# Performance work log

Hardware: AMD Instinct MI355X
Metric: run time of the kernel (lower is better)

## Reference

```python
import jax, jax.numpy as jnp
import numpy as np

B = 16
N = 1024            # num_nodes
U = 64              # num_units
K = 2               # max_diffusion_step
M = K + 1           # num diffusion matrices
F = 2 * U           # inputs + state features per node


def _random_walk(adj):
    # adj: [B, N, N]; faithful to torch: add I, degree = sum over dim 1 (column sums),
    # then diag_embed(d_inv) @ adj (scales rows).
    a = adj + jnp.eye(N, dtype=adj.dtype)
    d = jnp.sum(a, axis=1)                      # [B, N]
    d_inv = jnp.where(d == 0, jnp.zeros_like(d), 1.0 / d)
    return d_inv[:, :, None] * a                # [B, N, N]


def _diffuse(A, x):
    # Faithful reproduction of the torch concat pattern:
    xs = [x]
    if K > 0:
        x1 = jnp.matmul(A, x)
        xs.append(x1)
        for _ in range(2, K + 1):
            x2 = jnp.matmul(A, x1)
            xs.append(x1)
            x1 = x2
    return jnp.stack(xs, axis=-1)               # [B, N, F, M]


def _gconv(inputs, state, A0, A1, W0, b0, W1, b1):
    b = inputs.shape[0]
    x = jnp.concatenate([inputs.reshape(b, N, -1), state.reshape(b, N, -1)], axis=-1)  # [B,N,F]
    f = x.shape[-1]
    x0 = _diffuse(A0, x).reshape(b * N, f * M)
    x1 = _diffuse(A1, x).reshape(b * N, f * M)
    return (x0 @ W0 + b0) + (x1 @ W1 + b1)       # [B*N, out]


def setup_inputs() -> dict:
    key = jax.random.key(0)
    ks = jax.random.split(key, 12)
    din = F * M
    s = 1.0 / np.sqrt(din)
    inputs = jax.random.normal(ks[0], (B, N * U), dtype=jnp.float32)
    hx = jax.random.normal(ks[1], (B, N * U), dtype=jnp.float32)
    adj = jax.random.uniform(ks[2], (B, N, N), dtype=jnp.float32)
    W0 = jax.random.normal(ks[3], (din, 2 * U), dtype=jnp.float32) * s
    b0 = jnp.full((2 * U,), 0.1, dtype=jnp.float32)
    W1 = jax.random.normal(ks[4], (din, 2 * U), dtype=jnp.float32) * s
    b1 = jnp.full((2 * U,), 0.1, dtype=jnp.float32)
    Wc0 = jax.random.normal(ks[5], (din, U), dtype=jnp.float32) * s
    bc0 = jnp.full((U,), 0.1, dtype=jnp.float32)
    Wc1 = jax.random.normal(ks[6], (din, U), dtype=jnp.float32) * s
    bc1 = jnp.full((U,), 0.1, dtype=jnp.float32)
    return {"inputs": inputs, "hx": hx, "adj": adj, "W0": W0, "b0": b0,
            "W1": W1, "b1": b1, "Wc0": Wc0, "bc0": bc0, "Wc1": Wc1, "bc1": bc1}


def reference(inputs, hx, adj, W0, b0, W1, b1, Wc0, bc0, Wc1, bc1):
    b = inputs.shape[0]
    A0 = _random_walk(adj)
    A1 = _random_walk(jnp.transpose(adj, (0, 2, 1)))
    # reset / update gates
    value = jax.nn.sigmoid(_gconv(inputs, hx, A0, A1, W0, b0, W1, b1))  # [B*N, 2U]
    value = value.reshape(b, N, 2 * U)
    r = value[..., :U].reshape(b, N * U)
    u = value[..., U:].reshape(b, N * U)
    # candidate state
    c = _gconv(inputs, r * hx, A0, A1, Wc0, bc0, Wc1, bc1)              # [B*N, U]
    c = jnp.tanh(c).reshape(b, N * U)
    new_state = u * hx + (1.0 - u) * c
    return new_state
```

## Files before the change

kernel.cpp:

```cpp
#include <hip/hip_runtime.h>
#include <hip/hip_bf16.h>

typedef unsigned short u16;
typedef unsigned int u32;
typedef unsigned char u8;
typedef long i64;
typedef __bf16 bf16x8 __attribute__((ext_vector_type(8)));
typedef float floatx4 __attribute__((ext_vector_type(4)));

#define MFMA16(a,b,c) __builtin_amdgcn_mfma_f32_16x16x32_bf16((a),(b),(c),0,0,0)
#define MFMA8(a,b,c)  __builtin_amdgcn_mfma_f32_16x16x32_fp8_fp8((a),(b),(c),0,0,0)
#define AS1 __attribute__((address_space(1)))
#define AS3 __attribute__((address_space(3)))
#define VM6 asm volatile("s_waitcnt vmcnt(6)" ::: "memory")
#define VM4 asm volatile("s_waitcnt vmcnt(4)" ::: "memory")
#define VM3 asm volatile("s_waitcnt vmcnt(3)" ::: "memory")
#define VM2 asm volatile("s_waitcnt vmcnt(2)" ::: "memory")
#define VM0 asm volatile("s_waitcnt vmcnt(0)" ::: "memory")
#define SBAR __builtin_amdgcn_s_barrier()
#define SCHED0 __builtin_amdgcn_sched_barrier(0)

__device__ __forceinline__ void gl16(const void* g, void* l){
  __builtin_amdgcn_global_load_lds((const AS1 void*)g, (AS3 void*)l, 16, 0, 0);
}
__device__ __forceinline__ u16 f2bf(float f){
  u32 u = __builtin_bit_cast(u32, f);
  u += 0x7FFFu + ((u >> 16) & 1u);
  return (u16)(u >> 16);
}
__device__ __forceinline__ float bf2f(u16 h){
  u32 u = ((u32)h) << 16;
  return __builtin_bit_cast(float, u);
}
__device__ __forceinline__ bf16x8 ldfrag(const u16* p){
  return *(const bf16x8*)p;
}
__device__ __forceinline__ u32 pk4(float a, float b, float c, float d){
  int r = __builtin_amdgcn_cvt_pk_fp8_f32(a, b, 0, false);
  r = __builtin_amdgcn_cvt_pk_fp8_f32(c, d, r, true);
  return (u32)r;
}
__device__ __forceinline__ i64 ldA8(const char* chunk, int r, int kf, int lg){
  int sr = r >> 1;
  int G = (((r&1)<<2) + (kf<<1) + (lg>>1)) ^ (sr&7);
  return *(const i64*)(chunk + sr*128 + G*16 + (lg&1)*8);
}

__global__ __launch_bounds__(256) void kp3_prep(
    const float* __restrict__ inp, const float* __restrict__ hx,
    const float* __restrict__ adj,
    const float* __restrict__ W0, const float* __restrict__ b0,
    const float* __restrict__ W1, const float* __restrict__ b1,
    const float* __restrict__ Wc0, const float* __restrict__ bc0,
    const float* __restrict__ Wc1, const float* __restrict__ bc1,
    u16* __restrict__ WgT, u16* __restrict__ WcT,
    float* __restrict__ bias_g, float* __restrict__ bias_c,
    u8* __restrict__ adjf8, u8* __restrict__ adjTf8,
    u8* __restrict__ Xtf8, u16* __restrict__ XC2){
  __shared__ __align__(16) char sh[40960];
  int t = threadIdx.x;
  int blk = blockIdx.x;
  if (blk < 256) {
    float (*XT)[80] = (float(*)[80])sh;
    int r = t >> 2;
    int row = blk*64 + r;
    int fq = t & 3;
    const float4* ip = (const float4*)(inp + (size_t)row*64 + fq*16);
    const float4* hp = (const float4*)(hx  + (size_t)row*64 + fq*16);
    float iv[16], hv[16];
    #pragma unroll
    for (int q=0;q<4;q++){
      float4 a = ip[q]; iv[4*q]=a.x; iv[4*q+1]=a.y; iv[4*q+2]=a.z; iv[4*q+3]=a.w;
      float4 c = hp[q]; hv[4*q]=c.x; hv[4*q+1]=c.y; hv[4*q+2]=c.z; hv[4*q+3]=c.w;
    }
    u32 pi[8];
    #pragma unroll
    for (int q=0;q<8;q++)
      pi[q] = (u32)f2bf(iv[2*q]) | ((u32)f2bf(iv[2*q+1])<<16);
    size_t rbase = (size_t)row*384;
    *(uint4*)(XC2 + rbase + fq*16)     = make_uint4(pi[0],pi[1],pi[2],pi[3]);
    *(uint4*)(XC2 + rbase + fq*16 + 8) = make_uint4(pi[4],pi[5],pi[6],pi[7]);
    #pragma unroll
    for (int q=0;q<16;q++){
      XT[fq*16+q][r]    = iv[q];
      XT[64+fq*16+q][r] = hv[q];
    }
    __syncthreads();
    int feat = t >> 1, half = t & 1;
    int b = blk >> 4, n0 = (blk & 15)*64;
    const float* src = &XT[feat][half*32];
    u32 o[8];
    #pragma unroll
    for (int p=0;p<8;p++)
      o[p] = pk4(src[4*p],src[4*p+1],src[4*p+2],src[4*p+3]);
    u8* dst = Xtf8 + (size_t)b*131072 + (size_t)feat*1024 + n0 + half*32;
    *(uint4*)dst      = make_uint4(o[0],o[1],o[2],o[3]);
    *(uint4*)(dst+16) = make_uint4(o[4],o[5],o[6],o[7]);
    return;
  }
  if (blk < 544) {
    int id = (blk - 256)*256 + t;
    if (id < 128*384) {
      int n = id / 384, k = id % 384;
      float v;
      if (k < 128)       v = W0[(k*3+0)*128 + n] + W1[(k*3+0)*128 + n];
      else if (k < 256){ int f = k-128; v = W0[(f*3+1)*128+n] + W0[(f*3+2)*128+n]; }
      else             { int f = k-256; v = W1[(f*3+1)*128+n] + W1[(f*3+2)*128+n]; }
      WgT[(size_t)n*384 + k] = f2bf(v);
    } else {
      int id2 = id - 128*384;
      int n = id2 / 384, k = id2 % 384;
      float v;
      if (k < 128)       v = Wc0[(k*3+0)*64 + n] + Wc1[(k*3+0)*64 + n];
      else if (k < 256){ int f = k-128; v = Wc0[(f*3+1)*64+n] + Wc0[(f*3+2)*64+n]; }
      else             { int f = k-256; v = Wc1[(f*3+1)*64+n] + Wc1[(f*3+2)*64+n]; }
      WcT[(size_t)n*384 + k] = f2bf(v);
    }
    if (blk == 256) {
      if (t < 128) bias_g[t] = b0[t] + b1[t];
      if (t < 64)  bias_c[t] = bc0[t] + bc1[t];
    }
    return;
  }
  u8* ltb = (u8*)sh;
  int blk2 = blk - 544;
  int b = blk2 >> 6, st = (blk2 >> 2) & 15, h = blk2 & 3;
  int i0 = st*64;
  int r = t >> 2, cq = t & 3;
  size_t base = (size_t)b << 20;
  for (int c = h*4; c < h*4+4; ++c){
    int j0 = c*64, cb = c & 1;
    const float4* s4 = (const float4*)(adj + base + (size_t)(i0 + r)*1024 + j0 + (cq<<4));
    float v[16];
    #pragma unroll
    for (int q = 0; q < 4; q++) {
      float4 f = s4[q];
      v[4*q]=f.x; v[4*q+1]=f.y; v[4*q+2]=f.z; v[4*q+3]=f.w;
    }
    u32 pk[4];
    #pragma unroll
    for (int p = 0; p < 4; p++)
      pk[p] = pk4(v[4*p],v[4*p+1],v[4*p+2],v[4*p+3]);
    *(uint4*)(adjf8 + base + (size_t)(i0 + r)*1024 + j0 + (cq<<4)) =
      make_uint4(pk[0],pk[1],pk[2],pk[3]);
    #pragma unroll
    for (int q = 0; q < 16; q++)
      ltb[cb*4608 + (cq*16+q)*72 + r] = (u8)(pk[q>>2] >> ((q&3)*8));
    __syncthreads();
    u32 w4[4];
    #pragma unroll
    for (int p = 0; p < 4; p++){
      u32 b0v = ltb[cb*4608 + r*72 + cq*16 + 4*p];
      u32 b1v = ltb[cb*4608 + r*72 + cq*16 + 4*p+1];
      u32 b2v = ltb[cb*4608 + r*72 + cq*16 + 4*p+2];
      u32 b3v = ltb[cb*4608 + r*72 + cq*16 + 4*p+3];
      w4[p] = b0v | (b1v<<8) | (b2v<<16) | (b3v<<24);
    }
    *(uint4*)(adjTf8 + base + (size_t)(j0 + r)*1024 + i0 + (cq<<4)) =
      make_uint4(w4[0],w4[1],w4[2],w4[3]);
  }
}

__global__ __launch_bounds__(256) void kg2_gates(
    const u8* __restrict__ adjf8, const u8* __restrict__ adjTf8,
    const u8* __restrict__ Xtf8,
    const float* __restrict__ inp, const float* __restrict__ hx,
    const u16* __restrict__ WgT, const float* __restrict__ bias_g,
    u16* __restrict__ XC2, u8* __restrict__ Stf8, float* __restrict__ uBuf){
  __shared__ __align__(16) char lds[36864];
  int bid = ((blockIdx.x & 7)<<6) + (blockIdx.x >> 3);
  int mt = bid & 31, b = bid >> 5;
  int t = threadIdx.x, w = t>>6, l = t&63, lr = l&15, lg = l>>4;
  int wm = w>>1, wn = w&1;
  int gp = (l&7) ^ ((l>>3)&7);
  size_t off = (size_t)(2*(l>>3) + (gp>>2))*1024 + (gp&3)*16;
  const u8* A0g = adjf8  + ((size_t)b<<20) + (size_t)mt*32768 + off;
  const u8* A1g = adjTf8 + ((size_t)b<<20) + (size_t)mt*32768 + off;
  const u8* Bg  = Xtf8 + (size_t)b*131072 + off;
  floatx4 acc0[4] = {}, acc1[4] = {}, s0 = {}, s1 = {};
  const i64 ONES = 0x3838383838383838L;
  #define STG_KG(bufi, kk) do{ \
    if (w==0){ gl16(A0g+(kk), lds+(bufi)*2048); gl16(A0g+(kk)+16384, lds+(bufi)*2048+1024); gl16(Bg+(kk), lds+12288+(bufi)*8192); } \
    else if (w==1){ gl16(A1g+(kk), lds+6144+(bufi)*2048); gl16(A1g+(kk)+16384, lds+6144+(bufi)*2048+1024); gl16(Bg+(kk)+16384, lds+12288+(bufi)*8192+1024); } \
    else if (w==2){ gl16(Bg+(kk)+32768, lds+12288+(bufi)*8192+2048); gl16(Bg+(kk)+49152, lds+12288+(bufi)*8192+3072); gl16(Bg+(kk)+65536, lds+12288+(bufi)*8192+4096); } \
    else { gl16(Bg+(kk)+81920, lds+12288+(bufi)*8192+5120); gl16(Bg+(kk)+98304, lds+12288+(bufi)*8192+6144); gl16(Bg+(kk)+114688, lds+12288+(bufi)*8192+7168); } \
  }while(0)
  STG_KG(0, 0);
  STG_KG(1, 64);
  int cur = 0;
  for (int step = 0; step < 16; ++step){
    if (step < 14) {
      int nb = cur + 2; if (nb >= 3) nb -= 3;
      STG_KG(nb, (step+2)*64);
      VM6;
    } else if (step == 14) { VM3; } else { VM0; }
    SBAR; SCHED0;
    const char* A0b = lds + cur*2048;
    const char* A1b = lds + 6144 + cur*2048;
    const char* Bb  = lds + 12288 + cur*8192;
    #pragma unroll
    for (int kf=0; kf<2; kf++){
      i64 a0 = ldA8(A0b, wm*16+lr, kf, lg);
      i64 a1 = ldA8(A1b, wm*16+lr, kf, lg);
      s0 = MFMA8(a0, ONES, s0);
      s1 = MFMA8(a1, ONES, s1);
      #pragma unroll
      for (int nf=0; nf<4; nf++){
        i64 bb = ldA8(Bb, wn*64+nf*16+lr, kf, lg);
        acc0[nf] = MFMA8(a0, bb, acc0[nf]);
        acc1[nf] = MFMA8(a1, bb, acc1[nf]);
      }
    }
    SCHED0; SBAR;
    if (++cur == 3) cur = 0;
  }
  __syncthreads();
  u16* SL = (u16*)lds;
  u16* SLT = (u16*)(lds + 25088);
  float d0i[4], d1i[4];
  #pragma unroll
  for (int rr=0; rr<4; rr++){
    d1i[rr] = 1.0f / (s0[rr] + 1.0f);
    d0i[rr] = 1.0f / (s1[rr] + 1.0f);
  }
  #pragma unroll
  for (int nf = 0; nf < 4; nf++) {
    #pragma unroll
    for (int rr = 0; rr < 4; rr++) {
      int rl = wm*16 + lg*4 + rr;
      int row = mt*32 + rl;
      int col = wn*64 + nf*16 + lr;
      float xv = (col < 64) ? inp[(size_t)(b*1024+row)*64 + col]
                            : hx [(size_t)(b*1024+row)*64 + (col-64)];
      float y0 = (acc0[nf][rr] + xv) * d0i[rr];
      float y1 = (acc1[nf][rr] + xv) * d1i[rr];
      u16 b0v = f2bf(y0), b1v = f2bf(y1);
      SL[rl*392 + col]       = f2bf(xv);
      SL[rl*392 + 128 + col] = b0v;
      SL[rl*392 + 256 + col] = b1v;
      if (col < 64) {
        size_t grow = (size_t)(b*1024 + row)*384;
        XC2[grow + 128 + col] = b0v;
        XC2[grow + 256 + col] = b1v;
      }
    }
  }
  __syncthreads();
  floatx4 g[4] = {};
  for (int kk = 0; kk < 384; kk += 32) {
    int ko = kk + lg*8;
    bf16x8 a = ldfrag(&SL[(size_t)(wm*16+lr)*392 + ko]);
    #pragma unroll
    for (int nf = 0; nf < 4; nf++)
      g[nf] = MFMA16(a, ldfrag(WgT + (size_t)(wn*64+nf*16+lr)*384 + ko), g[nf]);
  }
  #pragma unroll
  for (int nf = 0; nf < 4; nf++) {
    #pragma unroll
    for (int rr = 0; rr < 4; rr++) {
      int rl = wm*16 + lg*4 + rr;
      int row = mt*32 + rl;
      int col = wn*64 + nf*16 + lr;
      float pre = g[nf][rr] + bias_g[col];
      float s = 1.0f / (1.0f + __expf(-pre));
      if (col < 64) {
        float shv = s * hx[(size_t)(b*1024+row)*64 + col];
        u16 bv = f2bf(shv);
        XC2[(size_t)(b*1024+row)*384 + 64 + col] = bv;
        SLT[col*40 + rl] = bv;
      } else {
        uBuf[(size_t)(b*1024+row)*64 + (col-64)] = s;
      }
    }
  }
  __syncthreads();
  {
    int c2 = t >> 2, q = t & 3;
    uint4 vv = *(const uint4*)&SLT[c2*40 + q*8];
    u32 arr[4] = {vv.x, vv.y, vv.z, vv.w};
    float f[8];
    #pragma unroll
    for (int e=0;e<8;e++) f[e] = bf2f((u16)(arr[e>>1] >> ((e&1)*16)));
    u32 p0 = pk4(f[0],f[1],f[2],f[3]);
    u32 p1 = pk4(f[4],f[5],f[6],f[7]);
    *(uint2*)(Stf8 + (size_t)b*65536 + (size_t)c2*1024 + mt*32 + q*8) = make_uint2(p0,p1);
  }
  #undef STG_KG
}

__global__ __launch_bounds__(256) void kz2_cand(
    const u8* __restrict__ adjf8, const u8* __restrict__ adjTf8,
    const u8* __restrict__ Stf8,
    const u16* __restrict__ XC2, const u16* __restrict__ WcT,
    const float* __restrict__ bias_c,
    const float* __restrict__ uBuf, const float* __restrict__ hx,
    float* __restrict__ out){
  __shared__ __align__(16) char lds[25088];
  int bid = ((blockIdx.x & 7)<<6) + (blockIdx.x >> 3);
  int mt = bid & 31, b = bid >> 5;
  int t = threadIdx.x, w = t>>6, l = t&63, lr = l&15, lg = l>>4;
  int wm = w>>1, wn = w&1;
  int gp = (l&7) ^ ((l>>3)&7);
  size_t off = (size_t)(2*(l>>3) + (gp>>2))*1024 + (gp&3)*16;
  const u8* A0g = adjf8  + ((size_t)b<<20) + (size_t)mt*32768 + off;
  const u8* A1g = adjTf8 + ((size_t)b<<20) + (size_t)mt*32768 + off;
  const u8* Bg  = Stf8 + (size_t)b*65536 + off;
  floatx4 z0[2] = {}, z1[2] = {}, s0 = {}, s1 = {};
  const i64 ONES = 0x3838383838383838L;
  #define STG_KZ(bufi, kk) do{ \
    if (w==0){ gl16(A0g+(kk), lds+(bufi)*2048); gl16(A0g+(kk)+16384, lds+(bufi)*2048+1024); } \
    else if (w==1){ gl16(A1g+(kk), lds+6144+(bufi)*2048); gl16(A1g+(kk)+16384, lds+6144+(bufi)*2048+1024); } \
    else if (w==2){ gl16(Bg+(kk), lds+12288+(bufi)*4096); gl16(Bg+(kk)+16384, lds+12288+(bufi)*4096+1024); } \
    else { gl16(Bg+(kk)+32768, lds+12288+(bufi)*4096+2048); gl16(Bg+(kk)+49152, lds+12288+(bufi)*4096+3072); } \
  }while(0)
  STG_KZ(0, 0);
  STG_KZ(1, 64);
  int cur = 0;
  for (int step = 0; step < 16; ++step){
    if (step < 14) {
      int nb = cur + 2; if (nb >= 3) nb -= 3;
      STG_KZ(nb, (step+2)*64);
      VM4;
    } else if (step == 14) { VM2; } else { VM0; }
    SBAR; SCHED0;
    const char* A0b = lds + cur*2048;
    const char* A1b = lds + 6144 + cur*2048;
    const char* Bb  = lds + 12288 + cur*4096;
    #pragma unroll
    for (int kf=0; kf<2; kf++){
      i64 a0 = ldA8(A0b, wm*16+lr, kf, lg);
      i64 a1 = ldA8(A1b, wm*16+lr, kf, lg);
      s0 = MFMA8(a0, ONES, s0);
      s1 = MFMA8(a1, ONES, s1);
      #pragma unroll
      for (int nf=0; nf<2; nf++){
        i64 bb = ldA8(Bb, wn*32+nf*16+lr, kf, lg);
        z0[nf] = MFMA8(a0, bb, z0[nf]);
        z1[nf] = MFMA8(a1, bb, z1[nf]);
      }
    }
    SCHED0; SBAR;
    if (++cur == 3) cur = 0;
  }
  __syncthreads();
  u16* SL = (u16*)lds;
  {
    int rl = t >> 3, s = t & 7;
    size_t grow = (size_t)(b*1024 + mt*32 + rl)*384;
    #pragma unroll
    for (int j = 0; j < 3; j++)
      *(uint4*)&SL[(size_t)rl*392 + s*24 + j*8] =
        *(const uint4*)(XC2 + grow + s*24 + j*8);
    *(uint4*)&SL[(size_t)rl*392 + 256 + s*8] =
      *(const uint4*)(XC2 + grow + 256 + s*8);
  }
  float d0i[4], d1i[4];
  #pragma unroll
  for (int rr=0; rr<4; rr++){
    d1i[rr] = 1.0f / (s0[rr] + 1.0f);
    d0i[rr] = 1.0f / (s1[rr] + 1.0f);
  }
  #pragma unroll
  for (int nf = 0; nf < 2; nf++) {
    #pragma unroll
    for (int rr = 0; rr < 4; rr++) {
      int rl = wm*16 + lg*4 + rr;
      int row = mt*32 + rl;
      int col = wn*32 + nf*16 + lr;
      float sval = bf2f(XC2[(size_t)(b*1024+row)*384 + 64 + col]);
      SL[rl*392 + 192 + col] = f2bf((z0[nf][rr] + sval) * d0i[rr]);
      SL[rl*392 + 320 + col] = f2bf((z1[nf][rr] + sval) * d1i[rr]);
    }
  }
  __syncthreads();
  floatx4 c[2] = {};
  for (int kk = 0; kk < 384; kk += 32) {
    int ko = kk + lg*8;
    bf16x8 a = ldfrag(&SL[(size_t)(wm*16+lr)*392 + ko]);
    #pragma unroll
    for (int nf = 0; nf < 2; nf++)
      c[nf] = MFMA16(a, ldfrag(WcT + (size_t)(wn*32+nf*16+lr)*384 + ko), c[nf]);
  }
  #pragma unroll
  for (int nf = 0; nf < 2; nf++) {
    #pragma unroll
    for (int rr = 0; rr < 4; rr++) {
      int row = mt*32 + wm*16 + lg*4 + rr;
      int col = wn*32 + nf*16 + lr;
      float pre = c[nf][rr] + bias_c[col];
      pre = fminf(fmaxf(pre, -15.f), 15.f);
      float e2 = __expf(2.0f*pre);
      float cv = (e2 - 1.0f) / (e2 + 1.0f);
      float u = uBuf[(size_t)(b*1024+row)*64 + col];
      float h = hx[(size_t)(b*1024+row)*64 + col];
      out[(size_t)(b*1024+row)*64 + col] = u*h + (1.0f - u)*cv;
    }
  }
  #undef STG_KZ
}

extern "C" void kernel_launch(void* const* d_in, const int* in_sizes, int n_in,
                              void* d_out, int out_size, void* d_ws, size_t ws_size,
                              hipStream_t stream) {
  (void)in_sizes; (void)n_in; (void)out_size; (void)ws_size;
  const float* inp = (const float*)d_in[0];
  const float* hx  = (const float*)d_in[1];
  const float* adj = (const float*)d_in[2];
  const float* W0  = (const float*)d_in[3];
  const float* b0  = (const float*)d_in[4];
  const float* W1  = (const float*)d_in[5];
  const float* b1  = (const float*)d_in[6];
  const float* Wc0 = (const float*)d_in[7];
  const float* bc0 = (const float*)d_in[8];
  const float* Wc1 = (const float*)d_in[9];
  const float* bc1 = (const float*)d_in[10];
  float* out = (float*)d_out;
  char* ws = (char*)d_ws;

  u8* adjf8   = (u8*)(ws + 0);
  u8* adjTf8  = (u8*)(ws + 16777216);
  u8* Xtf8    = (u8*)(ws + 33554432);
  u16* XC2    = (u16*)(ws + 35651584);
  u8* Stf8    = (u8*)(ws + 48234496);
  float* uBuf = (float*)(ws + 49283072);
  u16* WgT    = (u16*)(ws + 53477376);
  u16* WcT    = (u16*)(ws + 53575680);
  float* bias_g = (float*)(ws + 53624832);
  float* bias_c = (float*)(ws + 53625344);

  hipLaunchKernelGGL(kp3_prep, dim3(1568), dim3(256), 0, stream,
                     inp, hx, adj, W0, b0, W1, b1, Wc0, bc0, Wc1, bc1,
                     WgT, WcT, bias_g, bias_c, adjf8, adjTf8, Xtf8, XC2);
  hipLaunchKernelGGL(kg2_gates, dim3(512), dim3(256), 0, stream,
                     adjf8, adjTf8, Xtf8, inp, hx, WgT, bias_g, XC2, Stf8, uBuf);
  hipLaunchKernelGGL(kz2_cand, dim3(512), dim3(256), 0, stream,
                     adjf8, adjTf8, Stf8, XC2, WcT, bias_c, uBuf, hx, out);
}
```

Measured before the change: 74.83 us.

## Fuse prep, gate and candidate kernels into one cooperative persistent kernel

Replaces the three-launch pipeline (prep, gates, candidate) with one cooperative kernel of 512 blocks that uses grid.sync between phases. Intermediate per-tile data (the concatenated features, the update gate and the r*h values) stays in LDS across phases instead of round-tripping through global buffers such as XC2 and uBuf. This is meant to remove launch gaps and some global traffic. In exchange it adds two grid-wide barriers, requires all 512 blocks to be co-resident (2 per CU under the launch bounds), and falls back to the old three kernels if the cooperative launch fails.

```diff
diff --git a/kernel.cpp b/kernel.cpp
--- a/kernel.cpp
+++ b/kernel.cpp
@@ -1,5 +1,8 @@
 #include <hip/hip_runtime.h>
 #include <hip/hip_bf16.h>
+#include <hip/hip_cooperative_groups.h>
+
+namespace cg = cooperative_groups;
 
 typedef unsigned short u16;
 typedef unsigned int u32;
@@ -44,6 +47,308 @@
   int sr = r >> 1;
   int G = (((r&1)<<2) + (kf<<1) + (lg>>1)) ^ (sr&7);
   return *(const i64*)(chunk + sr*128 + G*16 + (lg&1)*8);
+}
+
+__global__ __launch_bounds__(256, 2) void mega(
+    const float* __restrict__ inp, const float* __restrict__ hx,
+    const float* __restrict__ adj,
+    const float* __restrict__ W0, const float* __restrict__ b0,
+    const float* __restrict__ W1, const float* __restrict__ b1,
+    const float* __restrict__ Wc0, const float* __restrict__ bc0,
+    const float* __restrict__ Wc1, const float* __restrict__ bc1,
+    u16* __restrict__ WgT, u16* __restrict__ WcT,
+    float* __restrict__ bias_g, float* __restrict__ bias_c,
+    u8* __restrict__ adjf8, u8* __restrict__ adjTf8,
+    u8* __restrict__ Xtf8, u8* __restrict__ Stf8,
+    float* __restrict__ out){
+  __shared__ __align__(16) char lds[53888];
+  cg::grid_group grid = cg::this_grid();
+  int t = threadIdx.x;
+  int blk = blockIdx.x;
+
+  if (blk < 256) {
+    float (*XT)[80] = (float(*)[80])lds;
+    int r = t >> 2, fq = t & 3;
+    int row = blk*64 + r;
+    const float4* ip = (const float4*)(inp + (size_t)row*64 + fq*16);
+    const float4* hp = (const float4*)(hx  + (size_t)row*64 + fq*16);
+    float iv[16], hv[16];
+    #pragma unroll
+    for (int q=0;q<4;q++){
+      float4 a = ip[q]; iv[4*q]=a.x; iv[4*q+1]=a.y; iv[4*q+2]=a.z; iv[4*q+3]=a.w;
+      float4 c = hp[q]; hv[4*q]=c.x; hv[4*q+1]=c.y; hv[4*q+2]=c.z; hv[4*q+3]=c.w;
+    }
+    #pragma unroll
+    for (int q=0;q<16;q++){
+      XT[fq*16+q][r]    = iv[q];
+      XT[64+fq*16+q][r] = hv[q];
+    }
+    __syncthreads();
+    int feat = t >> 1, half = t & 1;
+    int bb2 = blk >> 4, n0 = (blk & 15)*64;
+    const float* src = &XT[feat][half*32];
+    u32 o[8];
+    #pragma unroll
+    for (int p=0;p<8;p++)
+      o[p] = pk4(src[4*p],src[4*p+1],src[4*p+2],src[4*p+3]);
+    u8* dst = Xtf8 + (size_t)bb2*131072 + (size_t)feat*1024 + n0 + half*32;
+    *(uint4*)dst      = make_uint4(o[0],o[1],o[2],o[3]);
+    *(uint4*)(dst+16) = make_uint4(o[4],o[5],o[6],o[7]);
+    __syncthreads();
+  }
+  if (blk >= 224) {
+    int id = (blk - 224)*256 + t;
+    if (id < 128*384) {
+      int n = id / 384, k = id % 384;
+      float v;
+      if (k < 128)       v = W0[(k*3+0)*128 + n] + W1[(k*3+0)*128 + n];
+      else if (k < 256){ int f = k-128; v = W0[(f*3+1)*128+n] + W0[(f*3+2)*128+n]; }
+      else             { int f = k-256; v = W1[(f*3+1)*128+n] + W1[(f*3+2)*128+n]; }
+      WgT[(size_t)n*384 + k] = f2bf(v);
+    } else {
+      int id2 = id - 128*384;
+      int n = id2 / 384, k = id2 % 384;
+      float v;
+      if (k < 128)       v = Wc0[(k*3+0)*64 + n] + Wc1[(k*3+0)*64 + n];
+      else if (k < 256){ int f = k-128; v = Wc0[(f*3+1)*64+n] + Wc0[(f*3+2)*64+n]; }
+      else             { int f = k-256; v = Wc1[(f*3+1)*64+n] + Wc1[(f*3+2)*64+n]; }
+      WcT[(size_t)n*384 + k] = f2bf(v);
+    }
+    if (blk == 224) {
+      if (t < 128) bias_g[t] = b0[t] + b1[t];
+      if (t < 64)  bias_c[t] = bc0[t] + bc1[t];
+    }
+  }
+  {
+    u8* ltb = (u8*)lds;
+    int r = t >> 2, cq = t & 3;
+    for (int uu = blk*2; uu < blk*2 + 2; ++uu){
+      int b = uu >> 6, st = (uu >> 2) & 15, h = uu & 3;
+      int i0 = st*64;
+      size_t base = (size_t)b << 20;
+      __syncthreads();
+      for (int c = h*4; c < h*4+4; ++c){
+        int j0 = c*64, cb = c & 1;
+        const float4* s4 = (const float4*)(adj + base + (size_t)(i0 + r)*1024 + j0 + (cq<<4));
+        float v[16];
+        #pragma unroll
+        for (int q = 0; q < 4; q++) {
+          float4 f = s4[q];
+          v[4*q]=f.x; v[4*q+1]=f.y; v[4*q+2]=f.z; v[4*q+3]=f.w;
+        }
+        u32 pk[4];
+        #pragma unroll
+        for (int p = 0; p < 4; p++)
+          pk[p] = pk4(v[4*p],v[4*p+1],v[4*p+2],v[4*p+3]);
+        *(uint4*)(adjf8 + base + (size_t)(i0 + r)*1024 + j0 + (cq<<4)) =
+          make_uint4(pk[0],pk[1],pk[2],pk[3]);
+        #pragma unroll
+        for (int q = 0; q < 16; q++)
+          ltb[cb*4608 + (cq*16+q)*72 + r] = (u8)(pk[q>>2] >> ((q&3)*8));
+        __syncthreads();
+        u32 w4[4];
+        #pragma unroll
+        for (int p = 0; p < 4; p++){
+          u32 b0v = ltb[cb*4608 + r*72 + cq*16 + 4*p];
+          u32 b1v = ltb[cb*4608 + r*72 + cq*16 + 4*p+1];
+          u32 b2v = ltb[cb*4608 + r*72 + cq*16 + 4*p+2];
+          u32 b3v = ltb[cb*4608 + r*72 + cq*16 + 4*p+3];
+          w4[p] = b0v | (b1v<<8) | (b2v<<16) | (b3v<<24);
+        }
+        *(uint4*)(adjTf8 + base + (size_t)(j0 + r)*1024 + i0 + (cq<<4)) =
+          make_uint4(w4[0],w4[1],w4[2],w4[3]);
+      }
+    }
+  }
+  __threadfence();
+  grid.sync();
+
+  int bid = ((blk & 7)<<6) + (blk >> 3);
+  int mt = bid & 31, b = bid >> 5;
+  int w = t>>6, l = t&63, lr = l&15, lg = l>>4;
+  int wm = w>>1, wn = w&1;
+  int gp = (l&7) ^ ((l>>3)&7);
+  size_t off = (size_t)(2*(l>>3) + (gp>>2))*1024 + (gp&3)*16;
+  const u8* A0g = adjf8  + ((size_t)b<<20) + (size_t)mt*32768 + off;
+  const u8* A1g = adjTf8 + ((size_t)b<<20) + (size_t)mt*32768 + off;
+  u16* SL = (u16*)lds;
+  u16* uL = (u16*)(lds + 25088);
+  char* stg = lds + 29312;
+  const i64 ONES = 0x3838383838383838L;
+  float d0i[4], d1i[4];
+
+  {
+    const u8* Bg = Xtf8 + (size_t)b*131072 + off;
+    floatx4 acc0[4] = {}, acc1[4] = {}, s0 = {}, s1 = {};
+    #define STG_G(bi, kk) do{ \
+      if (w==0){ gl16(A0g+(kk), stg+(bi)*2048); gl16(A0g+(kk)+16384, stg+(bi)*2048+1024); gl16(Bg+(kk), stg+8192+(bi)*8192); } \
+      else if (w==1){ gl16(A1g+(kk), stg+4096+(bi)*2048); gl16(A1g+(kk)+16384, stg+4096+(bi)*2048+1024); gl16(Bg+(kk)+16384, stg+8192+(bi)*8192+1024); } \
+      else if (w==2){ gl16(Bg+(kk)+32768, stg+8192+(bi)*8192+2048); gl16(Bg+(kk)+49152, stg+8192+(bi)*8192+3072); gl16(Bg+(kk)+65536, stg+8192+(bi)*8192+4096); } \
+      else { gl16(Bg+(kk)+81920, stg+8192+(bi)*8192+5120); gl16(Bg+(kk)+98304, stg+8192+(bi)*8192+6144); gl16(Bg+(kk)+114688, stg+8192+(bi)*8192+7168); } \
+    }while(0)
+    STG_G(0, 0);
+    int cur = 0;
+    for (int step = 0; step < 16; ++step){
+      if (step < 15) { STG_G(cur^1, (step+1)*64); VM3; } else { VM0; }
+      SBAR; SCHED0;
+      const char* A0b = stg + cur*2048;
+      const char* A1b = stg + 4096 + cur*2048;
+      const char* Bb  = stg + 8192 + cur*8192;
+      #pragma unroll
+      for (int kf=0; kf<2; kf++){
+        i64 a0 = ldA8(A0b, wm*16+lr, kf, lg);
+        i64 a1 = ldA8(A1b, wm*16+lr, kf, lg);
+        s0 = MFMA8(a0, ONES, s0);
+        s1 = MFMA8(a1, ONES, s1);
+        #pragma unroll
+        for (int nf=0; nf<4; nf++){
+          i64 bb = ldA8(Bb, wn*64+nf*16+lr, kf, lg);
+          acc0[nf] = MFMA8(a0, bb, acc0[nf]);
+          acc1[nf] = MFMA8(a1, bb, acc1[nf]);
+        }
+      }
+      SCHED0; SBAR;
+      cur ^= 1;
+    }
+    #undef STG_G
+    __syncthreads();
+    #pragma unroll
+    for (int rr=0; rr<4; rr++){
+      d1i[rr] = 1.0f / (s0[rr] + 1.0f);
+      d0i[rr] = 1.0f / (s1[rr] + 1.0f);
+    }
+    #pragma unroll
+    for (int nf = 0; nf < 4; nf++) {
+      #pragma unroll
+      for (int rr = 0; rr < 4; rr++) {
+        int rl = wm*16 + lg*4 + rr;
+        int row = mt*32 + rl;
+        int col = wn*64 + nf*16 + lr;
+        float xv = (col < 64) ? inp[(size_t)(b*1024+row)*64 + col]
+                              : hx [(size_t)(b*1024+row)*64 + (col-64)];
+        float y0 = (acc0[nf][rr] + xv) * d0i[rr];
+        float y1 = (acc1[nf][rr] + xv) * d1i[rr];
+        SL[rl*392 + col]       = f2bf(xv);
+        SL[rl*392 + 128 + col] = f2bf(y0);
+        SL[rl*392 + 256 + col] = f2bf(y1);
+      }
+    }
+    __syncthreads();
+    floatx4 g[4] = {};
+    for (int kk = 0; kk < 384; kk += 32) {
+      int ko = kk + lg*8;
+      bf16x8 a = ldfrag(&SL[(size_t)(wm*16+lr)*392 + ko]);
+      #pragma unroll
+      for (int nf = 0; nf < 4; nf++)
+        g[nf] = MFMA16(a, ldfrag(WgT + (size_t)(wn*64+nf*16+lr)*384 + ko), g[nf]);
+    }
+    __syncthreads();
+    u16* SLT = (u16*)stg;
+    #pragma unroll
+    for (int nf = 0; nf < 4; nf++) {
+      #pragma unroll
+      for (int rr = 0; rr < 4; rr++) {
+        int rl = wm*16 + lg*4 + rr;
+        int row = mt*32 + rl;
+        int col = wn*64 + nf*16 + lr;
+        float pre = g[nf][rr] + bias_g[col];
+        float s = 1.0f / (1.0f + __expf(-pre));
+        if (col < 64) {
+          float shv = s * hx[(size_t)(b*1024+row)*64 + col];
+          u16 bv = f2bf(shv);
+          SL[rl*392 + 64 + col] = bv;
+          SLT[col*40 + rl] = bv;
+        } else {
+          uL[rl*66 + (col-64)] = f2bf(s);
+        }
+      }
+    }
+    __syncthreads();
+    {
+      int c2 = t >> 2, q = t & 3;
+      uint4 vv = *(const uint4*)&SLT[c2*40 + q*8];
+      u32 arr[4] = {vv.x, vv.y, vv.z, vv.w};
+      float f[8];
+      #pragma unroll
+      for (int e=0;e<8;e++) f[e] = bf2f((u16)(arr[e>>1] >> ((e&1)*16)));
+      u32 p0 = pk4(f[0],f[1],f[2],f[3]);
+      u32 p1 = pk4(f[4],f[5],f[6],f[7]);
+      *(uint2*)(Stf8 + (size_t)b*65536 + (size_t)c2*1024 + mt*32 + q*8) = make_uint2(p0,p1);
+    }
+  }
+  __threadfence();
+  grid.sync();
+
+  {
+    const u8* Bg = Stf8 + (size_t)b*65536 + off;
+    floatx4 z0[2] = {}, z1[2] = {};
+    #define STG_Z(bi, kk) do{ \
+      if (w==0){ gl16(A0g+(kk), stg+(bi)*2048); gl16(A0g+(kk)+16384, stg+(bi)*2048+1024); } \
+      else if (w==1){ gl16(A1g+(kk), stg+4096+(bi)*2048); gl16(A1g+(kk)+16384, stg+4096+(bi)*2048+1024); } \
+      else if (w==2){ gl16(Bg+(kk), stg+8192+(bi)*4096); gl16(Bg+(kk)+16384, stg+8192+(bi)*4096+1024); } \
+      else { gl16(Bg+(kk)+32768, stg+8192+(bi)*4096+2048); gl16(Bg+(kk)+49152, stg+8192+(bi)*4096+3072); } \
+    }while(0)
+    STG_Z(0, 0);
+    int cur = 0;
+    for (int step = 0; step < 16; ++step){
+      if (step < 15) { STG_Z(cur^1, (step+1)*64); VM2; } else { VM0; }
+      SBAR; SCHED0;
+      const char* A0b = stg + cur*2048;
+      const char* A1b = stg + 4096 + cur*2048;
+      const char* Bb  = stg + 8192 + cur*4096;
+      #pragma unroll
+      for (int kf=0; kf<2; kf++){
+        i64 a0 = ldA8(A0b, wm*16+lr, kf, lg);
+        i64 a1 = ldA8(A1b, wm*16+lr, kf, lg);
+        #pragma unroll
+        for (int nf=0; nf<2; nf++){
+          i64 bb = ldA8(Bb, wn*32+nf*16+lr, kf, lg);
+          z0[nf] = MFMA8(a0, bb, z0[nf]);
+          z1[nf] = MFMA8(a1, bb, z1[nf]);
+        }
+      }
+      SCHED0; SBAR;
+      cur ^= 1;
+    }
+    #undef STG_Z
+    __syncthreads();
+    #pragma unroll
+    for (int nf = 0; nf < 2; nf++) {
+      #pragma unroll
+      for (int rr = 0; rr < 4; rr++) {
+        int rl = wm*16 + lg*4 + rr;
+        int col = wn*32 + nf*16 + lr;
+        float sval = bf2f(SL[rl*392 + 64 + col]);
+        SL[rl*392 + 192 + col] = f2bf((z0[nf][rr] + sval) * d0i[rr]);
+        SL[rl*392 + 320 + col] = f2bf((z1[nf][rr] + sval) * d1i[rr]);
+      }
+    }
+    __syncthreads();
+    floatx4 c[2] = {};
+    for (int kk = 0; kk < 384; kk += 32) {
+      int ko = kk + lg*8;
+      bf16x8 a = ldfrag(&SL[(size_t)(wm*16+lr)*392 + ko]);
+      #pragma unroll
+      for (int nf = 0; nf < 2; nf++)
+        c[nf] = MFMA16(a, ldfrag(WcT + (size_t)(wn*32+nf*16+lr)*384 + ko), c[nf]);
+    }
+    #pragma unroll
+    for (int nf = 0; nf < 2; nf++) {
+      #pragma unroll
+      for (int rr = 0; rr < 4; rr++) {
+        int rl = wm*16 + lg*4 + rr;
+        int row = mt*32 + rl;
+        int col = wn*32 + nf*16 + lr;
+        float pre = c[nf][rr] + bias_c[col];
+        pre = fminf(fmaxf(pre, -15.f), 15.f);
+        float e2 = __expf(2.0f*pre);
+        float cv = (e2 - 1.0f) / (e2 + 1.0f);
+        float u = bf2f(uL[rl*66 + col]);
+        float h = hx[(size_t)(b*1024+row)*64 + col];
+        out[(size_t)(b*1024+row)*64 + col] = u*h + (1.0f - u)*cv;
+      }
+    }
+  }
 }
 
 __global__ __launch_bounds__(256) void kp3_prep(
@@ -62,9 +367,8 @@
   int blk = blockIdx.x;
   if (blk < 256) {
     float (*XT)[80] = (float(*)[80])sh;
-    int r = t >> 2;
+    int r = t >> 2, fq = t & 3;
     int row = blk*64 + r;
-    int fq = t & 3;
     const float4* ip = (const float4*)(inp + (size_t)row*64 + fq*16);
     const float4* hp = (const float4*)(hx  + (size_t)row*64 + fq*16);
     float iv[16], hv[16];
@@ -428,11 +732,18 @@
   float* bias_g = (float*)(ws + 53624832);
   float* bias_c = (float*)(ws + 53625344);
 
-  hipLaunchKernelGGL(kp3_prep, dim3(1568), dim3(256), 0, stream,
-                     inp, hx, adj, W0, b0, W1, b1, Wc0, bc0, Wc1, bc1,
-                     WgT, WcT, bias_g, bias_c, adjf8, adjTf8, Xtf8, XC2);
-  hipLaunchKernelGGL(kg2_gates, dim3(512), dim3(256), 0, stream,
-                     adjf8, adjTf8, Xtf8, inp, hx, WgT, bias_g, XC2, Stf8, uBuf);
-  hipLaunchKernelGGL(kz2_cand, dim3(512), dim3(256), 0, stream,
-                     adjf8, adjTf8, Stf8, XC2, WcT, bias_c, uBuf, hx, out);
-}
+  void* args[] = {&inp, &hx, &adj, &W0, &b0, &W1, &b1, &Wc0, &bc0, &Wc1, &bc1,
+                  &WgT, &WcT, &bias_g, &bias_c, &adjf8, &adjTf8, &Xtf8, &Stf8,
+                  &out};
+  hipError_t e = hipLaunchCooperativeKernel((void*)mega, dim3(512), dim3(256),
+                                            args, 0, stream);
+  if (e != hipSuccess) {
+    hipLaunchKernelGGL(kp3_prep, dim3(1568), dim3(256), 0, stream,
+                       inp, hx, adj, W0, b0, W1, b1, Wc0, bc0, Wc1, bc1,
+                       WgT, WcT, bias_g, bias_c, adjf8, adjTf8, Xtf8, XC2);
+    hipLaunchKernelGGL(kg2_gates, dim3(512), dim3(256), 0, stream,
+                       adjf8, adjTf8, Xtf8, inp, hx, WgT, bias_g, XC2, Stf8, uBuf);
+    hipLaunchKernelGGL(kz2_cand, dim3(512), dim3(256), 0, stream,
+                       adjf8, adjTf8, Stf8, XC2, WcT, bias_c, uBuf, hx, out);
+  }
+}
```

Result: slower. 292.3 us (+290.7%).
